# Performance work log

Hardware: AMD Instinct MI355X
Metric: run time of the kernel (lower is better)

The kernel has to match this reference:

```python
import jax, jax.numpy as jnp
import numpy as np

N_DAYS, N_HOURS, N_LINKS, N_FEATS = 4, 24, 2000, 4
N_PATHS, N_ODS = 20000, 4000
EPS = 1e-12


def setup_inputs() -> dict:
    key = jax.random.key(0)
    ks = jax.random.split(key, 9)
    # X: (days, hours, links, 1 + n_features); channel 0 is free-flow travel time tt_ff
    X = jax.random.uniform(ks[0], (N_DAYS, N_HOURS, N_LINKS, N_FEATS + 1), dtype=jnp.float32) + 0.1
    # utility coefficients; signs '-' for all cost features (projected via clip to <= 0)
    theta_raw = -jax.random.uniform(ks[1], (N_FEATS,), dtype=jnp.float32)
    theta_links = 0.01 * jax.random.normal(ks[2], (N_LINKS,), dtype=jnp.float32)
    q_sqrt = jax.random.uniform(ks[3], (N_ODS,), dtype=jnp.float32) + 0.5  # q = q_sqrt**2
    log_alpha = 0.1 * jax.random.normal(ks[4], (N_LINKS,), dtype=jnp.float32)
    beta_raw = jax.random.uniform(ks[5], (N_LINKS,), dtype=jnp.float32, minval=1.0, maxval=3.0)
    k = jax.random.uniform(ks[6], (N_LINKS,), dtype=jnp.float32, minval=50.0, maxval=150.0)
    # link-path incidence D (n_links, n_paths), ~10 links per path
    D = (jax.random.uniform(ks[7], (N_LINKS, N_PATHS)) < 0.005).astype(jnp.float32)
    # OD segment id of each path (sorted, one OD per path) == sparse M structure
    od_of_path = jnp.sort(jax.random.randint(ks[8], (N_PATHS,), 0, N_ODS, dtype=jnp.int32))
    return dict(X=X, theta_raw=theta_raw, theta_links=theta_links, q_sqrt=q_sqrt,
                log_alpha=log_alpha, beta_raw=beta_raw, k=k, D=D,
                od_of_path=od_of_path, n_ods=N_ODS)


def reference(X, theta_raw, theta_links, q_sqrt, log_alpha, beta_raw, k, D, od_of_path, n_ods):
    # project_theta: all features have sign '-', so clip to (-inf, 0]
    theta = jnp.minimum(theta_raw, 0.0)
    tt_ff = X[..., 0]              # (d, h, l)
    feats = X[..., 1:]             # (d, h, l, f)
    # link utilities: einsum('ijkl,l->ijk') + theta_links
    V = jnp.einsum('dhlf,f->dhl', feats, theta) + theta_links
    # path utilities: einsum('ijk,kl->ijl') with D (links, paths)
    vf = jnp.einsum('dhl,lp->dhp', V, D)            # (d, h, p)
    vf_t = jnp.moveaxis(vf, -1, 0)                  # (p, d, h) paths leading for segment ops
    # segmented softmax over paths within each OD choice set (sparse M pattern)
    vmax = jax.lax.stop_gradient(
        jax.ops.segment_max(vf_t, od_of_path, num_segments=n_ods))   # (ods, d, h)
    ev = jnp.exp(vf_t - vmax[od_of_path])
    denom = jax.ops.segment_sum(ev, od_of_path, num_segments=n_ods)[od_of_path]
    pf = ev / denom                                  # (p, d, h) path probabilities
    # path flows: pf scaled by OD demand q = q_sqrt**2
    q = q_sqrt ** 2
    f = pf * q[od_of_path][:, None, None]            # (p, d, h)
    # link flows + relu
    x = jax.nn.relu(jnp.einsum('pdh,lp->dhl', f, D))  # (d, h, l)
    # BPR link travel times: tt_ff * (1 + alpha * (x/k)^beta)
    alpha = jnp.exp(log_alpha)
    beta = jnp.clip(beta_raw, EPS, 4.0)
    return tt_ff * (1.0 + alpha * jnp.power(x / k, beta))
```

## Files before the change

kernel.cpp:

```cpp
#include <hip/hip_runtime.h>
#include <math.h>

#define NDH 96
#define ND4 24
#define NL  2000
#define NP  20000
#define NOD 4000
#define PL_CAP 32
#define LP_CAP 150
#define LP_LDS 256

typedef unsigned short u16;
typedef unsigned int   u32;
typedef u32 v4u __attribute__((ext_vector_type(4)));

__device__ __forceinline__ int lower_bound_od(const int* __restrict__ od, int key) {
    int lo = 0, hi = NP;
    while (lo < hi) { int mid = (lo + hi) >> 1; if (od[mid] < key) lo = mid + 1; else hi = mid; }
    return lo;
}

__global__ __launch_bounds__(256) void kBV(const float* __restrict__ D,
                                           const float* __restrict__ X,
                                           const float* __restrict__ theta_raw,
                                           const float* __restrict__ theta_links,
                                           const int* __restrict__ od,
                                           float* __restrict__ V,
                                           int* __restrict__ start,
                                           int* __restrict__ lc,
                                           u16* __restrict__ lp,
                                           int* __restrict__ pc,
                                           u16* __restrict__ pl) {
    __shared__ u16 slp[LP_LDS];
    __shared__ int scnt;
    int l = blockIdx.x;
    int tid = threadIdx.x;
    if (tid == 0) scnt = 0;

    if (tid < NDH) {
        float t0 = fminf(theta_raw[0], 0.f);
        float t1 = fminf(theta_raw[1], 0.f);
        float t2 = fminf(theta_raw[2], 0.f);
        float t3 = fminf(theta_raw[3], 0.f);
        const float* xp = X + ((size_t)(tid * NL + l)) * 5;
        V[l * NDH + tid] = theta_links[l]
                         + t0 * xp[1] + t1 * xp[2] + t2 * xp[3] + t3 * xp[4];
    } else if (tid < 98) {
        int sid = l * 2 + (tid - 96);
        start[sid] = lower_bound_od(od, sid);
    } else if (tid == 98 && l == 0) {
        start[NOD] = lower_bound_od(od, NOD);
    }
    __syncthreads();

    const v4u* row4 = (const v4u*)(D + (size_t)l * NP);
    for (int base = 0; base < 5000; base += 2048) {
        v4u v[8];
        int idx[8];
#pragma unroll
        for (int k = 0; k < 8; k++) {
            idx[k] = base + k * 256 + tid;
            if (idx[k] < 5000) {
                v[k] = __builtin_nontemporal_load(row4 + idx[k]);
            } else {
                v[k][0] = 0u; v[k][1] = 0u; v[k][2] = 0u; v[k][3] = 0u;
            }
        }
#pragma unroll
        for (int k = 0; k < 8; k++) {
            if ((v[k][0] | v[k][1] | v[k][2] | v[k][3]) == 0u) continue;
            int p0 = idx[k] * 4;
            if (v[k][0]) { int s = atomicAdd(&scnt, 1); if (s < LP_LDS) slp[s] = (u16)(p0);     }
            if (v[k][1]) { int s = atomicAdd(&scnt, 1); if (s < LP_LDS) slp[s] = (u16)(p0 + 1); }
            if (v[k][2]) { int s = atomicAdd(&scnt, 1); if (s < LP_LDS) slp[s] = (u16)(p0 + 2); }
            if (v[k][3]) { int s = atomicAdd(&scnt, 1); if (s < LP_LDS) slp[s] = (u16)(p0 + 3); }
        }
    }
    __syncthreads();
    int c = min(scnt, LP_CAP);
    for (int j = tid; j < c; j += 256) {
        int p = (int)slp[j];
        lp[l * LP_CAP + j] = (u16)p;
        int s = atomicAdd(&pc[p], 1);
        if (s < PL_CAP) pl[p * PL_CAP + s] = (u16)l;
    }
    if (tid == 0) lc[l] = scnt;
}

__global__ __launch_bounds__(256) void kDE(const float* __restrict__ V,
                                           const int* __restrict__ pc,
                                           const u16* __restrict__ pl,
                                           const int* __restrict__ start,
                                           const float* __restrict__ q_sqrt,
                                           float* __restrict__ vf) {
    int t = blockIdx.x * blockDim.x + threadIdx.x;
    if (t >= NOD * ND4) return;
    int o = t / ND4, d4 = t - o * ND4;
    int a = start[o], b = start[o + 1];
    if (a >= b) return;
    const float4* V4 = (const float4*)V;
    float4* vf4 = (float4*)vf;

    float4 m = make_float4(-INFINITY, -INFINITY, -INFINITY, -INFINITY);
    float4 s = make_float4(0.f, 0.f, 0.f, 0.f);
    for (int p = a; p < b; p++) {
        int c = min(pc[p], PL_CAP);
        const u16* plrow = pl + p * PL_CAP;
        float4 acc = make_float4(0.f, 0.f, 0.f, 0.f);
        for (int j0 = 0; j0 < c; j0 += 8) {
            int li[8];
#pragma unroll
            for (int q = 0; q < 8; q++) li[q] = (j0 + q < c) ? (int)plrow[j0 + q] : -1;
#pragma unroll
            for (int q = 0; q < 8; q++) {
                if (li[q] >= 0) {
                    float4 v = V4[li[q] * ND4 + d4];
                    acc.x += v.x; acc.y += v.y; acc.z += v.z; acc.w += v.w;
                }
            }
        }
        vf4[p * ND4 + d4] = acc;
        float4 mn;
        mn.x = fmaxf(m.x, acc.x); mn.y = fmaxf(m.y, acc.y);
        mn.z = fmaxf(m.z, acc.z); mn.w = fmaxf(m.w, acc.w);
        s.x = s.x * expf(m.x - mn.x) + expf(acc.x - mn.x);
        s.y = s.y * expf(m.y - mn.y) + expf(acc.y - mn.y);
        s.z = s.z * expf(m.z - mn.z) + expf(acc.z - mn.z);
        s.w = s.w * expf(m.w - mn.w) + expf(acc.w - mn.w);
        m = mn;
    }
    float q = q_sqrt[o]; float qq = q * q;
    float4 rs = make_float4(qq / s.x, qq / s.y, qq / s.z, qq / s.w);
    for (int p = a; p < b; p++) {
        float4 v = vf4[p * ND4 + d4];
        v.x = expf(v.x - m.x) * rs.x; v.y = expf(v.y - m.y) * rs.y;
        v.z = expf(v.z - m.z) * rs.z; v.w = expf(v.w - m.w) * rs.w;
        vf4[p * ND4 + d4] = v;
    }
}

__global__ __launch_bounds__(192) void kF4(const float* __restrict__ f,
                                           const int* __restrict__ lc,
                                           const u16* __restrict__ lp,
                                           const float* __restrict__ X,
                                           const float* __restrict__ log_alpha,
                                           const float* __restrict__ beta_raw,
                                           const float* __restrict__ kk,
                                           float* __restrict__ out) {
    __shared__ float4 sf[8 * ND4];
    __shared__ u16 slp2[LP_CAP];
    int l  = blockIdx.x;
    int c  = min(lc[l], LP_CAP);
    for (int j = threadIdx.x; j < c; j += 192) slp2[j] = lp[l * LP_CAP + j];
    __syncthreads();
    int d4 = threadIdx.x % ND4;
    int jc = threadIdx.x / ND4;
    const float4* f4 = (const float4*)f;
    float4 acc = make_float4(0.f, 0.f, 0.f, 0.f);
    for (int j0 = jc; j0 < c; j0 += 32) {
        int jj[4];
#pragma unroll
        for (int t = 0; t < 4; t++) {
            int j = j0 + t * 8;
            jj[t] = (j < c) ? (int)slp2[j] : -1;
        }
#pragma unroll
        for (int t = 0; t < 4; t++) {
            if (jj[t] >= 0) {
                float4 v = f4[jj[t] * ND4 + d4];
                acc.x += v.x; acc.y += v.y; acc.z += v.z; acc.w += v.w;
            }
        }
    }
    sf[jc * ND4 + d4] = acc;
    __syncthreads();
    if (jc == 0) {
        float4 t = sf[d4];
#pragma unroll
        for (int r = 1; r < 8; r++) {
            float4 u = sf[r * ND4 + d4];
            t.x += u.x; t.y += u.y; t.z += u.z; t.w += u.w;
        }
        float alpha = expf(log_alpha[l]);
        float beta  = fminf(fmaxf(beta_raw[l], 1e-12f), 4.0f);
        float kv    = kk[l];
        float xs[4] = { t.x, t.y, t.z, t.w };
#pragma unroll
        for (int k4 = 0; k4 < 4; k4++) {
            int dh = d4 * 4 + k4;
            float xv = fmaxf(xs[k4], 0.f);
            float tt = X[((size_t)(dh * NL + l)) * 5];
            out[dh * NL + l] = tt * (1.0f + alpha * powf(xv / kv, beta));
        }
    }
}

extern "C" void kernel_launch(void* const* d_in, const int* in_sizes, int n_in,
                              void* d_out, int out_size, void* d_ws, size_t ws_size,
                              hipStream_t stream) {
    const float* X           = (const float*)d_in[0];
    const float* theta_raw   = (const float*)d_in[1];
    const float* theta_links = (const float*)d_in[2];
    const float* q_sqrt      = (const float*)d_in[3];
    const float* log_alpha   = (const float*)d_in[4];
    const float* beta_raw    = (const float*)d_in[5];
    const float* kk          = (const float*)d_in[6];
    const float* D           = (const float*)d_in[7];
    const int*   od          = (const int*)d_in[8];
    float* out = (float*)d_out;
    char* ws = (char*)d_ws;

    int*   pc    = (int*)(ws + 0);
    int*   lc    = (int*)(ws + 80000);
    int*   start = (int*)(ws + 88064);
    float* V     = (float*)(ws + 104576);
    u16*   pl    = (u16*)(ws + 872576);
    u16*   lp    = (u16*)(ws + 2152576);
    float* vf    = (float*)(ws + 2785024);

    hipMemsetAsync(pc, 0, 80000, stream);

    kBV <<<NL, 256, 0, stream>>>(D, X, theta_raw, theta_links, od, V, start, lc, lp, pc, pl);
    kDE <<<(NOD * ND4 + 255) / 256, 256, 0, stream>>>(V, pc, pl, start, q_sqrt, vf);
    kF4 <<<NL, 192, 0, stream>>>(vf, lc, lp, X, log_alpha, beta_raw, kk, out);
}
```

Baseline: 315.4 us.

## Parallelize per-OD softmax across paths with one block per OD

Replaces the thread-per-(OD, time-quad) kernel, which walked every path of an OD serially, with a block per OD. Up to 10 paths are gathered in parallel by groups of 24 threads, and their sums are merged into an online max/sum kept in shared memory. When an OD has 10 or fewer paths, the path utilities stay in shared memory, so the vf write and re-read round trip is skipped. The cost is 4000 blocks where only 240 of 256 threads do useful work, several block-wide barriers, and a serial merge done by 24 threads.

```diff
diff --git a/kernel.cpp b/kernel.cpp
--- a/kernel.cpp
+++ b/kernel.cpp
@@ -9,6 +9,7 @@
 #define PL_CAP 32
 #define LP_CAP 150
 #define LP_LDS 256
+#define WPATH 10
 
 typedef unsigned short u16;
 typedef unsigned int   u32;
@@ -87,55 +88,99 @@
     if (tid == 0) lc[l] = scnt;
 }
 
-__global__ __launch_bounds__(256) void kDE(const float* __restrict__ V,
-                                           const int* __restrict__ pc,
-                                           const u16* __restrict__ pl,
-                                           const int* __restrict__ start,
-                                           const float* __restrict__ q_sqrt,
-                                           float* __restrict__ vf) {
-    int t = blockIdx.x * blockDim.x + threadIdx.x;
-    if (t >= NOD * ND4) return;
-    int o = t / ND4, d4 = t - o * ND4;
+__global__ __launch_bounds__(256) void kDE2(const float* __restrict__ V,
+                                            const int* __restrict__ pc,
+                                            const u16* __restrict__ pl,
+                                            const int* __restrict__ start,
+                                            const float* __restrict__ q_sqrt,
+                                            float* __restrict__ vf) {
+    __shared__ float4 wacc[WPATH][ND4];
+    __shared__ float4 m4[ND4];
+    __shared__ float4 s4[ND4];
+    __shared__ float4 rs4[ND4];
+    int o = blockIdx.x;
     int a = start[o], b = start[o + 1];
     if (a >= b) return;
+    int tid = threadIdx.x;
+    int pw  = tid / ND4;
+    int d4  = tid - pw * ND4;
     const float4* V4 = (const float4*)V;
     float4* vf4 = (float4*)vf;
-
-    float4 m = make_float4(-INFINITY, -INFINITY, -INFINITY, -INFINITY);
-    float4 s = make_float4(0.f, 0.f, 0.f, 0.f);
-    for (int p = a; p < b; p++) {
-        int c = min(pc[p], PL_CAP);
-        const u16* plrow = pl + p * PL_CAP;
-        float4 acc = make_float4(0.f, 0.f, 0.f, 0.f);
-        for (int j0 = 0; j0 < c; j0 += 8) {
-            int li[8];
-#pragma unroll
-            for (int q = 0; q < 8; q++) li[q] = (j0 + q < c) ? (int)plrow[j0 + q] : -1;
-#pragma unroll
-            for (int q = 0; q < 8; q++) {
-                if (li[q] >= 0) {
-                    float4 v = V4[li[q] * ND4 + d4];
-                    acc.x += v.x; acc.y += v.y; acc.z += v.z; acc.w += v.w;
+    int np = b - a;
+    bool single = (np <= WPATH);
+
+    if (tid < ND4) {
+        m4[tid] = make_float4(-INFINITY, -INFINITY, -INFINITY, -INFINITY);
+        s4[tid] = make_float4(0.f, 0.f, 0.f, 0.f);
+    }
+    __syncthreads();
+
+    for (int w0 = a; w0 < b; w0 += WPATH) {
+        int p = w0 + pw;
+        if (pw < WPATH && p < b) {
+            int c = min(pc[p], PL_CAP);
+            const u16* plrow = pl + p * PL_CAP;
+            float4 acc = make_float4(0.f, 0.f, 0.f, 0.f);
+            for (int j0 = 0; j0 < c; j0 += 8) {
+                int li[8];
+#pragma unroll
+                for (int q = 0; q < 8; q++) li[q] = (j0 + q < c) ? (int)plrow[j0 + q] : -1;
+#pragma unroll
+                for (int q = 0; q < 8; q++) {
+                    if (li[q] >= 0) {
+                        float4 v = V4[li[q] * ND4 + d4];
+                        acc.x += v.x; acc.y += v.y; acc.z += v.z; acc.w += v.w;
+                    }
                 }
             }
-        }
-        vf4[p * ND4 + d4] = acc;
-        float4 mn;
-        mn.x = fmaxf(m.x, acc.x); mn.y = fmaxf(m.y, acc.y);
-        mn.z = fmaxf(m.z, acc.z); mn.w = fmaxf(m.w, acc.w);
-        s.x = s.x * expf(m.x - mn.x) + expf(acc.x - mn.x);
-        s.y = s.y * expf(m.y - mn.y) + expf(acc.y - mn.y);
-        s.z = s.z * expf(m.z - mn.z) + expf(acc.z - mn.z);
-        s.w = s.w * expf(m.w - mn.w) + expf(acc.w - mn.w);
-        m = mn;
-    }
-    float q = q_sqrt[o]; float qq = q * q;
-    float4 rs = make_float4(qq / s.x, qq / s.y, qq / s.z, qq / s.w);
-    for (int p = a; p < b; p++) {
-        float4 v = vf4[p * ND4 + d4];
-        v.x = expf(v.x - m.x) * rs.x; v.y = expf(v.y - m.y) * rs.y;
-        v.z = expf(v.z - m.z) * rs.z; v.w = expf(v.w - m.w) * rs.w;
-        vf4[p * ND4 + d4] = v;
+            if (!single) vf4[p * ND4 + d4] = acc;
+            wacc[pw][d4] = acc;
+        }
+        __syncthreads();
+        if (tid < ND4) {
+            float4 m = m4[tid], s = s4[tid];
+            int lim = min(WPATH, b - w0);
+            for (int i = 0; i < lim; i++) {
+                float4 v = wacc[i][tid];
+                float4 nm;
+                nm.x = fmaxf(m.x, v.x); nm.y = fmaxf(m.y, v.y);
+                nm.z = fmaxf(m.z, v.z); nm.w = fmaxf(m.w, v.w);
+                s.x = s.x * expf(m.x - nm.x) + expf(v.x - nm.x);
+                s.y = s.y * expf(m.y - nm.y) + expf(v.y - nm.y);
+                s.z = s.z * expf(m.z - nm.z) + expf(v.z - nm.z);
+                s.w = s.w * expf(m.w - nm.w) + expf(v.w - nm.w);
+                m = nm;
+            }
+            m4[tid] = m; s4[tid] = s;
+        }
+        __syncthreads();
+    }
+
+    if (tid < ND4) {
+        float q = q_sqrt[o]; float qq = q * q;
+        float4 s = s4[tid];
+        rs4[tid] = make_float4(qq / s.x, qq / s.y, qq / s.z, qq / s.w);
+    }
+    __syncthreads();
+
+    float4 m = m4[d4], rs = rs4[d4];
+    if (single) {
+        int p = a + pw;
+        if (pw < WPATH && p < b) {
+            float4 v = wacc[pw][d4];
+            float4 f;
+            f.x = expf(v.x - m.x) * rs.x; f.y = expf(v.y - m.y) * rs.y;
+            f.z = expf(v.z - m.z) * rs.z; f.w = expf(v.w - m.w) * rs.w;
+            vf4[p * ND4 + d4] = f;
+        }
+    } else if (pw < WPATH) {
+        for (int p = a + pw; p < b; p += WPATH) {
+            float4 v = vf4[p * ND4 + d4];
+            float4 f;
+            f.x = expf(v.x - m.x) * rs.x; f.y = expf(v.y - m.y) * rs.y;
+            f.z = expf(v.z - m.z) * rs.z; f.w = expf(v.w - m.w) * rs.w;
+            vf4[p * ND4 + d4] = f;
+        }
     }
 }
 
@@ -221,6 +266,6 @@
     hipMemsetAsync(pc, 0, 80000, stream);
 
     kBV <<<NL, 256, 0, stream>>>(D, X, theta_raw, theta_links, od, V, start, lc, lp, pc, pl);
-    kDE <<<(NOD * ND4 + 255) / 256, 256, 0, stream>>>(V, pc, pl, start, q_sqrt, vf);
+    kDE2<<<NOD, 256, 0, stream>>>(V, pc, pl, start, q_sqrt, vf);
     kF4 <<<NL, 192, 0, stream>>>(vf, lc, lp, X, log_alpha, beta_raw, kk, out);
 }
```

Result: faster. 288.8 us (-8.4%).
